# Optimization experiments

Measured on AMD Instinct MI355X. Metric: run time of the kernel, lower is better.

## Reference

```python
import jax, jax.numpy as jnp
import numpy as np

LN_EPS = 1e-5

def _layernorm(x, w, b):
    mu = jnp.mean(x, axis=-1, keepdims=True)
    var = jnp.mean(jnp.square(x - mu), axis=-1, keepdims=True)
    return (x - mu) * jax.lax.rsqrt(var + LN_EPS) * w + b

def setup_inputs() -> dict:
    key = jax.random.key(0)
    ks = jax.random.split(key, 6)
    B, NQ, QD = 8, 576, 4096
    NKV, KVD = 2304, 1024
    s = 0.02
    return {
        "x_q": jax.random.normal(ks[0], (B, NQ, QD), jnp.float32),
        "x_kv": jax.random.normal(ks[1], (B, NKV, KVD), jnp.float32),
        "q_ln_w": jnp.ones((QD,), jnp.float32),
        "q_ln_b": jnp.zeros((QD,), jnp.float32),
        "q_w": jax.random.normal(ks[2], (QD, QD), jnp.float32) * s,
        "q_b": jnp.zeros((QD,), jnp.float32),
        "k_ln_w": jnp.ones((KVD,), jnp.float32),
        "k_ln_b": jnp.zeros((KVD,), jnp.float32),
        "k_w": jax.random.normal(ks[3], (KVD, QD), jnp.float32) * s,
        "k_b": jnp.zeros((QD,), jnp.float32),
        "v_ln_w": jnp.ones((KVD,), jnp.float32),
        "v_ln_b": jnp.zeros((KVD,), jnp.float32),
        "v_w": jax.random.normal(ks[4], (KVD, QD), jnp.float32) * s,
        "v_b": jnp.zeros((QD,), jnp.float32),
    }

def reference(x_q, x_kv, q_ln_w, q_ln_b, q_w, q_b,
              k_ln_w, k_ln_b, k_w, k_b, v_ln_w, v_ln_b, v_w, v_b):
    B, NQ, QD = x_q.shape
    hw = int(round(x_kv.shape[1] ** 0.5))          # 48
    KVD = x_kv.shape[-1]
    patch_num = int(round(NQ ** 0.5))              # 24
    patch_size = hw // patch_num                   # 2
    # 'b (h w) d -> b h w d' then group into patch_num x patch_num windows
    kv = x_kv.reshape(B, hw, hw, KVD)
    kv = kv.reshape(B, patch_num, patch_size, patch_num, patch_size, KVD)
    kv = kv.transpose(0, 1, 3, 2, 4, 5).reshape(B, patch_num * patch_num, patch_size * patch_size, KVD)
    # projections (LayerNorm + Linear)
    q = _layernorm(x_q, q_ln_w, q_ln_b) @ q_w + q_b            # [B, P2, QD]
    k = _layernorm(kv, k_ln_w, k_ln_b) @ k_w + k_b             # [B, P2, S2, QD]
    v = _layernorm(kv, v_ln_w, v_ln_b) @ v_w + v_b             # [B, P2, S2, QD]
    scale = 1.0 / (QD ** 0.5)
    att = jnp.einsum('bpd,bpsd->bps', q, k) * scale            # [B, P2, S2]
    att = jnp.nan_to_num(att)
    att = jax.nn.softmax(att, axis=-1)
    feat = jnp.einsum('bps,bpsd->bpd', att, v)                 # [B, P2, QD]
    return (x_q, feat)
```

## Files before the change

kernel.cpp:

```cpp
#include <hip/hip_runtime.h>
#include <cstdint>
#include <cstddef>


typedef __attribute__((ext_vector_type(8))) short short8;
typedef __attribute__((ext_vector_type(4))) float f32x4;

#define DEV __device__ __forceinline__

DEV unsigned short f2bf(float f) {
  union { float f; unsigned u; } x; x.f = f;
  unsigned r = x.u + 0x7fffu + ((x.u >> 16) & 1u);
  return (unsigned short)(r >> 16);
}
DEV float bf2f(unsigned short u) {
  union { unsigned u; float f; } x; x.u = ((unsigned)u) << 16;
  return x.f;
}

DEV void gload16(const void* g, void* l) {
  __builtin_amdgcn_global_load_lds(
      (const __attribute__((address_space(1))) unsigned int*)g,
      (__attribute__((address_space(3))) unsigned int*)l, 16, 0, 0);
}

template <bool PARTIAL, bool HAS_BIAS>
__global__ __launch_bounds__(512, 2) void gemm_nt(
    const unsigned short* __restrict__ A, const unsigned short* __restrict__ Bm,
    void* __restrict__ Cv, const float* __restrict__ bias, int M, int N,
    int Kfull, int Kchunk) {
  __shared__ __align__(16) unsigned short lds_a[2][256 * 64];
  __shared__ __align__(16) unsigned short lds_b[2][256 * 64];
  const int t = threadIdx.x;
  const int l = t & 63;
  const int wid = t >> 6;

  int bx = blockIdx.x, by = blockIdx.y;
  {
    const int nbx = gridDim.x, nby = gridDim.y;
    const int nwg = nbx * nby;
    int flat = by * nbx + bx;
    flat = (flat & 7) * (nwg >> 3) + (flat >> 3);
    bx = flat % nbx;
    by = flat / nbx;
  }
  const long brow = (long)bx * 256;
  const long bcol = (long)by * 256;
  const int z = blockIdx.z;
  const int k0 = z * Kchunk;

  const int srow0 = t >> 3;
  const int gsrc = (t & 7) ^ ((t >> 3) & 7);
  const unsigned short* aS[4];
  const unsigned short* bS[4];
#pragma unroll
  for (int j = 0; j < 4; ++j) {
    const long row = srow0 + 64 * j;
    aS[j] = A + (brow + row) * (long)Kfull + k0 + gsrc * 8;
    bS[j] = Bm + (bcol + row) * (long)Kfull + k0 + gsrc * 8;
  }
  const int dOff = t * 8;

  const int wr = wid >> 2, wc = wid & 3;
  const int fr = l & 15;
  const int xr = fr & 7;
  const int gq0 = l >> 4;

  f32x4 acc[8][4] = {};

#pragma unroll
  for (int j = 0; j < 4; ++j) {
    gload16(aS[j], &lds_a[0][dOff + 4096 * j]);
    gload16(bS[j], &lds_b[0][dOff + 4096 * j]);
  }
  asm volatile("s_waitcnt vmcnt(0)" ::: "memory");
  __syncthreads();

  int cur = 0;
  for (int kt = 0; kt < Kchunk; kt += 64) {
    const int nxt = cur ^ 1;
    if (kt + 64 < Kchunk) {
#pragma unroll
      for (int j = 0; j < 4; ++j) {
        gload16(aS[j] + kt + 64, &lds_a[nxt][dOff + 4096 * j]);
        gload16(bS[j] + kt + 64, &lds_b[nxt][dOff + 4096 * j]);
      }
    }
#pragma unroll
    for (int ks = 0; ks < 2; ++ks) {
      const int gx = ((ks * 4 + gq0) ^ xr) * 8;
      short8 bfr[4];
#pragma unroll
      for (int ni = 0; ni < 4; ++ni)
        bfr[ni] =
            *(const short8*)&lds_b[cur][(wc * 64 + ni * 16 + fr) * 64 + gx];
#pragma unroll
      for (int mi = 0; mi < 8; ++mi) {
        const short8 af =
            *(const short8*)&lds_a[cur][(wr * 128 + mi * 16 + fr) * 64 + gx];
#pragma unroll
        for (int ni = 0; ni < 4; ++ni)
          acc[mi][ni] = __builtin_amdgcn_mfma_f32_16x16x32_bf16(
              af, bfr[ni], acc[mi][ni], 0, 0, 0);
      }
    }
    asm volatile("s_waitcnt vmcnt(0)" ::: "memory");
    __syncthreads();
    cur = nxt;
  }

  const int crow = (l >> 4) * 4;
  unsigned short* Cpart =
      PARTIAL ? ((unsigned short*)Cv + (size_t)z * M * (size_t)N) : nullptr;
#pragma unroll
  for (int ni = 0; ni < 4; ++ni) {
    const long col = bcol + wc * 64 + ni * 16 + fr;
    const float bv = (!PARTIAL && HAS_BIAS) ? bias[col] : 0.0f;
#pragma unroll
    for (int mi = 0; mi < 8; ++mi) {
#pragma unroll
      for (int r = 0; r < 4; ++r) {
        const long row = brow + wr * 128 + mi * 16 + crow + r;
        const float v = acc[mi][ni][r] + bv;
        if (PARTIAL)
          Cpart[row * (long)N + col] = f2bf(v);
        else
          ((float*)Cv)[row * (long)N + col] = v;
      }
    }
  }
}

__global__ __launch_bounds__(256) void reduce_splits_bf16(
    const unsigned short* __restrict__ part, unsigned short* __restrict__ out,
    int S, size_t MN) {
  size_t i = (size_t)blockIdx.x * 256 + threadIdx.x;
  const size_t n4 = MN / 4;
  const size_t stride = (size_t)gridDim.x * 256;
  for (; i < n4; i += stride) {
    float a0 = 0.f, a1 = 0.f, a2 = 0.f, a3 = 0.f;
    for (int s = 0; s < S; ++s) {
      const ushort4 b = ((const ushort4*)(part + (size_t)s * MN))[i];
      a0 += bf2f(b.x); a1 += bf2f(b.y); a2 += bf2f(b.z); a3 += bf2f(b.w);
    }
    ((ushort4*)out)[i] = make_ushort4(f2bf(a0), f2bf(a1), f2bf(a2), f2bf(a3));
  }
}

__global__ __launch_bounds__(256) void ln_q_kernel(
    const float* __restrict__ x, const float* __restrict__ w,
    const float* __restrict__ b, float* __restrict__ copy_out,
    unsigned short* __restrict__ qn) {
  const int row = blockIdx.x, t = threadIdx.x;
  const float4* xr = (const float4*)(x + (size_t)row * 4096);
  float4 v[4];
  float s = 0.f, s2 = 0.f;
#pragma unroll
  for (int j = 0; j < 4; ++j) {
    v[j] = xr[j * 256 + t];
    s += v[j].x + v[j].y + v[j].z + v[j].w;
    s2 += v[j].x * v[j].x + v[j].y * v[j].y + v[j].z * v[j].z + v[j].w * v[j].w;
  }
#pragma unroll
  for (int off = 32; off; off >>= 1) {
    s += __shfl_xor(s, off);
    s2 += __shfl_xor(s2, off);
  }
  __shared__ float red[8];
  if ((t & 63) == 0) { red[t >> 6] = s; red[4 + (t >> 6)] = s2; }
  __syncthreads();
  s = red[0] + red[1] + red[2] + red[3];
  s2 = red[4] + red[5] + red[6] + red[7];
  const float mu = s * (1.f / 4096.f);
  const float rstd = rsqrtf(s2 * (1.f / 4096.f) - mu * mu + 1e-5f);
  float4* co = (float4*)(copy_out + (size_t)row * 4096);
  unsigned short* qr = qn + (size_t)row * 4096;
#pragma unroll
  for (int j = 0; j < 4; ++j) {
    co[j * 256 + t] = v[j];
    const int c = (j * 256 + t) * 4;
    const float4 wv = *(const float4*)(w + c);
    const float4 bv = *(const float4*)(b + c);
    ushort4 o = make_ushort4(f2bf((v[j].x - mu) * rstd * wv.x + bv.x),
                             f2bf((v[j].y - mu) * rstd * wv.y + bv.y),
                             f2bf((v[j].z - mu) * rstd * wv.z + bv.z),
                             f2bf((v[j].w - mu) * rstd * wv.w + bv.w));
    *(ushort4*)(qr + c) = o;
  }
}

__global__ __launch_bounds__(256) void ln_kv_kernel(
    const float* __restrict__ x, unsigned short* __restrict__ h) {
  const int row = blockIdx.x, t = threadIdx.x;
  const float4 v = ((const float4*)(x + (size_t)row * 1024))[t];
  float s = v.x + v.y + v.z + v.w;
  float s2 = v.x * v.x + v.y * v.y + v.z * v.z + v.w * v.w;
#pragma unroll
  for (int off = 32; off; off >>= 1) {
    s += __shfl_xor(s, off);
    s2 += __shfl_xor(s2, off);
  }
  __shared__ float red[8];
  if ((t & 63) == 0) { red[t >> 6] = s; red[4 + (t >> 6)] = s2; }
  __syncthreads();
  s = red[0] + red[1] + red[2] + red[3];
  s2 = red[4] + red[5] + red[6] + red[7];
  const float mu = s * (1.f / 1024.f);
  const float rstd = rsqrtf(s2 * (1.f / 1024.f) - mu * mu + 1e-5f);
  *(ushort4*)(h + (size_t)row * 1024 + t * 4) =
      make_ushort4(f2bf((v.x - mu) * rstd), f2bf((v.y - mu) * rstd),
                   f2bf((v.z - mu) * rstd), f2bf((v.w - mu) * rstd));
}

__global__ __launch_bounds__(256) void conv_bf16(
    const float* __restrict__ src, unsigned short* __restrict__ dst, int n4) {
  int i = blockIdx.x * 256 + threadIdx.x;
  const int stride = gridDim.x * 256;
  for (; i < n4; i += stride) {
    const float4 v = ((const float4*)src)[i];
    ((ushort4*)dst)[i] = make_ushort4(f2bf(v.x), f2bf(v.y), f2bf(v.z), f2bf(v.w));
  }
}

__global__ __launch_bounds__(256) void conv_kw_qkb(
    const float* __restrict__ kw, const float* __restrict__ qb,
    unsigned short* __restrict__ kwb, float* __restrict__ qkb) {
  const int c = blockIdx.x, t = threadIdx.x;
  const float4* kr = (const float4*)(kw + (size_t)c * 4096);
  const float4* q4 = (const float4*)qb;
  ushort4* ko = (ushort4*)(kwb + (size_t)c * 4096);
  float s = 0.f;
#pragma unroll
  for (int j = 0; j < 4; ++j) {
    const float4 a = q4[j * 256 + t], b = kr[j * 256 + t];
    ko[j * 256 + t] = make_ushort4(f2bf(b.x), f2bf(b.y), f2bf(b.z), f2bf(b.w));
    s += a.x * b.x + a.y * b.y + a.z * b.z + a.w * b.w;
  }
#pragma unroll
  for (int off = 32; off; off >>= 1) s += __shfl_xor(s, off);
  __shared__ float red[4];
  if ((t & 63) == 0) red[t >> 6] = s;
  __syncthreads();
  if (t == 0) qkb[c] = red[0] + red[1] + red[2] + red[3];
}

__global__ void transpose_conv(const float* __restrict__ src,
                               const float* __restrict__ vlnw,
                               unsigned short* __restrict__ dst) {
  __shared__ float tile[32][33];
  const int n0 = blockIdx.x * 32, k0 = blockIdx.y * 32;
  const int tx = threadIdx.x, ty = threadIdx.y;
#pragma unroll
  for (int i = 0; i < 32; i += 8)
    tile[ty + i][tx] = src[(size_t)(k0 + ty + i) * 4096 + n0 + tx];
  __syncthreads();
  const float vw_ = vlnw[k0 + tx];
#pragma unroll
  for (int i = 0; i < 32; i += 8)
    dst[(size_t)(n0 + ty + i) * 1024 + k0 + tx] = f2bf(tile[tx][ty + i] * vw_);
}

__global__ __launch_bounds__(256) void vb_fold(const float* __restrict__ vw_,
                                               const float* __restrict__ vlnb,
                                               const float* __restrict__ vb,
                                               float* __restrict__ bias2) {
  const int nl = threadIdx.x & 63;
  const int seg = threadIdx.x >> 6;
  const int n = blockIdx.x * 64 + nl;
  float s = 0.f;
  for (int d = seg * 256; d < seg * 256 + 256; ++d)
    s += vlnb[d] * vw_[(size_t)d * 4096 + n];
  __shared__ float red[4][64];
  red[seg][nl] = s;
  __syncthreads();
  if (seg == 0)
    bias2[n] = vb[n] + red[0][nl] + red[1][nl] + red[2][nl] + red[3][nl];
}

__global__ __launch_bounds__(256) void att_fused(
    const unsigned short* __restrict__ part, int S, size_t PMN,
    const float* __restrict__ qkb, const float* __restrict__ klnw,
    const unsigned short* __restrict__ h, unsigned short* __restrict__ mix) {
  const int m = blockIdx.x;
  const int b = m / 576, p = m % 576;
  const int py = p / 24, px = p % 24;
  const int t = threadIdx.x, w = t >> 6, l = t & 63;
  const int c = t * 4;
  const size_t off = (size_t)m * 1024 + c;

  float4 q = *(const float4*)(qkb + c);
  for (int s = 0; s < S; ++s) {
    const ushort4 pp = *(const ushort4*)(part + (size_t)s * PMN + off);
    q.x += bf2f(pp.x); q.y += bf2f(pp.y); q.z += bf2f(pp.z); q.w += bf2f(pp.w);
  }
  const float4 kw4 = *(const float4*)(klnw + c);
  q.x *= kw4.x; q.y *= kw4.y; q.z *= kw4.z; q.w *= kw4.w;

  size_t rows[4];
#pragma unroll
  for (int s = 0; s < 4; ++s)
    rows[s] = ((size_t)b * 2304 + (size_t)(py * 2 + (s >> 1)) * 48 +
               (px * 2 + (s & 1))) * 1024;

  float hv[4][4];
  float dot[4];
#pragma unroll
  for (int s = 0; s < 4; ++s) {
    const ushort4 h4 = *(const ushort4*)(h + rows[s] + c);
    hv[s][0] = bf2f(h4.x); hv[s][1] = bf2f(h4.y);
    hv[s][2] = bf2f(h4.z); hv[s][3] = bf2f(h4.w);
    dot[s] = q.x * hv[s][0] + q.y * hv[s][1] + q.z * hv[s][2] + q.w * hv[s][3];
  }
#pragma unroll
  for (int s = 0; s < 4; ++s)
#pragma unroll
    for (int o = 32; o; o >>= 1) dot[s] += __shfl_xor(dot[s], o);

  __shared__ float red[4][4];
  if (l == 0) {
#pragma unroll
    for (int s = 0; s < 4; ++s) red[w][s] = dot[s];
  }
  __syncthreads();
  float lg[4];
#pragma unroll
  for (int s = 0; s < 4; ++s)
    lg[s] = (red[0][s] + red[1][s] + red[2][s] + red[3][s]) * 0.015625f;
  const float mx = fmaxf(fmaxf(lg[0], lg[1]), fmaxf(lg[2], lg[3]));
  float e[4];
#pragma unroll
  for (int s = 0; s < 4; ++s) e[s] = __expf(lg[s] - mx);
  const float inv = 1.f / (e[0] + e[1] + e[2] + e[3]);

  float a0 = 0.f, a1 = 0.f, a2 = 0.f, a3 = 0.f;
#pragma unroll
  for (int s = 0; s < 4; ++s) {
    const float at = e[s] * inv;
    a0 += at * hv[s][0];
    a1 += at * hv[s][1];
    a2 += at * hv[s][2];
    a3 += at * hv[s][3];
  }
  *(ushort4*)(mix + off) =
      make_ushort4(f2bf(a0), f2bf(a1), f2bf(a2), f2bf(a3));
}

extern "C" void kernel_launch(void* const* d_in, const int* in_sizes, int n_in,
                              void* d_out, int out_size, void* d_ws,
                              size_t ws_size, hipStream_t stream) {
  const float* x_q = (const float*)d_in[0];
  const float* x_kv = (const float*)d_in[1];
  const float* q_ln_w = (const float*)d_in[2];
  const float* q_ln_b = (const float*)d_in[3];
  const float* q_w = (const float*)d_in[4];
  const float* q_b = (const float*)d_in[5];
  const float* k_ln_w = (const float*)d_in[6];
  const float* k_w = (const float*)d_in[8];
  const float* v_ln_w = (const float*)d_in[10];
  const float* v_ln_b = (const float*)d_in[11];
  const float* v_w = (const float*)d_in[12];
  const float* v_b = (const float*)d_in[13];

  char* ws = (char*)d_ws;
  unsigned short* qn = (unsigned short*)(ws);
  unsigned short* h = (unsigned short*)(ws + 37748736);
  float* bias2 = (float*)(ws + 75497472);
  unsigned short* qwb = (unsigned short*)(ws + 113246208);
  unsigned short* kwb = (unsigned short*)(ws + 146800640);
  unsigned short* Wt = (unsigned short*)(ws + 155189248);
  unsigned short* vwT = (unsigned short*)(ws + 163577856);
  float* qkbv = (float*)(ws + 190840832);
  unsigned short* mix = (unsigned short*)(ws + 190844928);
  unsigned short* part = (unsigned short*)(ws + 200282112);

  const size_t MN_W = (size_t)1024 * 4096;
  const size_t MN_QK = (size_t)4608 * 1024;
  int splitW = 1, splitQK = 1;
  if (ws_size >= 200282112ull + 4 * MN_QK * 2) { splitW = 4; splitQK = 4; }
  else if (ws_size >= 200282112ull + 2 * MN_QK * 2) { splitW = 2; splitQK = 2; }

  float* out0 = (float*)d_out;
  float* out1 = out0 + (size_t)4608 * 4096;

  ln_q_kernel<<<4608, 256, 0, stream>>>(x_q, q_ln_w, q_ln_b, out0, qn);
  ln_kv_kernel<<<18432, 256, 0, stream>>>(x_kv, h);
  conv_bf16<<<4096, 256, 0, stream>>>(q_w, qwb, 4096 * 4096 / 4);
  conv_kw_qkb<<<1024, 256, 0, stream>>>(k_w, q_b, kwb, qkbv);
  transpose_conv<<<dim3(128, 32), dim3(32, 8), 0, stream>>>(v_w, v_ln_w, vwT);
  vb_fold<<<64, 256, 0, stream>>>(v_w, v_ln_b, v_b, bias2);

  gemm_nt<true, false><<<dim3(4, 16, splitW), 512, 0, stream>>>(
      kwb, qwb, part, nullptr, 1024, 4096, 4096, 4096 / splitW);
  reduce_splits_bf16<<<2048, 256, 0, stream>>>(part, Wt, splitW, MN_W);

  gemm_nt<true, false><<<dim3(18, 4, splitQK), 512, 0, stream>>>(
      qn, Wt, part, nullptr, 4608, 1024, 4096, 4096 / splitQK);
  att_fused<<<4608, 256, 0, stream>>>(part, splitQK, MN_QK, qkbv, k_ln_w, h,
                                      mix);

  gemm_nt<false, true><<<dim3(18, 16, 1), 512, 0, stream>>>(
      mix, vwT, out1, bias2, 4608, 4096, 1024, 1024);
}
```

Before: 599.5 us.

## Shrink GEMM tiles to 128x128 with 4 waves and single-buffered LDS

The GEMM kernel moves from 256x256 tiles with 8 waves and double-buffered LDS to 128x128 tiles with 4 waves and a single LDS buffer. Each tile now loads, waits and then computes, with no prefetch. The grids grow accordingly, and the W-product split-K drops from 4 to 2. The aim is more workgroups and higher occupancy per CU, at the cost of less data reuse per tile and exposed global-load latency.

```diff
diff --git a/kernel.cpp b/kernel.cpp
--- a/kernel.cpp
+++ b/kernel.cpp
@@ -25,15 +25,15 @@
 }
 
 template <bool PARTIAL, bool HAS_BIAS>
-__global__ __launch_bounds__(512, 2) void gemm_nt(
+__global__ __launch_bounds__(256, 2) void gemm_nt(
     const unsigned short* __restrict__ A, const unsigned short* __restrict__ Bm,
     void* __restrict__ Cv, const float* __restrict__ bias, int M, int N,
     int Kfull, int Kchunk) {
-  __shared__ __align__(16) unsigned short lds_a[2][256 * 64];
-  __shared__ __align__(16) unsigned short lds_b[2][256 * 64];
+  __shared__ __align__(16) unsigned short lds_a[128 * 64];
+  __shared__ __align__(16) unsigned short lds_b[128 * 64];
   const int t = threadIdx.x;
   const int l = t & 63;
-  const int wid = t >> 6;
+  const int w = t >> 6;
 
   int bx = blockIdx.x, by = blockIdx.y;
   {
@@ -44,8 +44,8 @@
     bx = flat % nbx;
     by = flat / nbx;
   }
-  const long brow = (long)bx * 256;
-  const long bcol = (long)by * 256;
+  const long brow = (long)bx * 128;
+  const long bcol = (long)by * 128;
   const int z = blockIdx.z;
   const int k0 = z * Kchunk;
 
@@ -53,60 +53,50 @@
   const int gsrc = (t & 7) ^ ((t >> 3) & 7);
   const unsigned short* aS[4];
   const unsigned short* bS[4];
+  unsigned short* aD[4];
+  unsigned short* bD[4];
 #pragma unroll
   for (int j = 0; j < 4; ++j) {
-    const long row = srow0 + 64 * j;
+    const long row = srow0 + 32 * j;
     aS[j] = A + (brow + row) * (long)Kfull + k0 + gsrc * 8;
     bS[j] = Bm + (bcol + row) * (long)Kfull + k0 + gsrc * 8;
-  }
-  const int dOff = t * 8;
-
-  const int wr = wid >> 2, wc = wid & 3;
+    aD[j] = lds_a + (t + 256 * j) * 8;
+    bD[j] = lds_b + (t + 256 * j) * 8;
+  }
+
+  const int wr = w >> 1, wc = w & 1;
   const int fr = l & 15;
   const int xr = fr & 7;
   const int gq0 = l >> 4;
 
-  f32x4 acc[8][4] = {};
-
-#pragma unroll
-  for (int j = 0; j < 4; ++j) {
-    gload16(aS[j], &lds_a[0][dOff + 4096 * j]);
-    gload16(bS[j], &lds_b[0][dOff + 4096 * j]);
-  }
-  asm volatile("s_waitcnt vmcnt(0)" ::: "memory");
-  __syncthreads();
-
-  int cur = 0;
+  f32x4 acc[4][4] = {};
+
   for (int kt = 0; kt < Kchunk; kt += 64) {
-    const int nxt = cur ^ 1;
-    if (kt + 64 < Kchunk) {
-#pragma unroll
-      for (int j = 0; j < 4; ++j) {
-        gload16(aS[j] + kt + 64, &lds_a[nxt][dOff + 4096 * j]);
-        gload16(bS[j] + kt + 64, &lds_b[nxt][dOff + 4096 * j]);
-      }
-    }
-#pragma unroll
-    for (int ks = 0; ks < 2; ++ks) {
-      const int gx = ((ks * 4 + gq0) ^ xr) * 8;
-      short8 bfr[4];
-#pragma unroll
-      for (int ni = 0; ni < 4; ++ni)
-        bfr[ni] =
-            *(const short8*)&lds_b[cur][(wc * 64 + ni * 16 + fr) * 64 + gx];
-#pragma unroll
-      for (int mi = 0; mi < 8; ++mi) {
-        const short8 af =
-            *(const short8*)&lds_a[cur][(wr * 128 + mi * 16 + fr) * 64 + gx];
-#pragma unroll
-        for (int ni = 0; ni < 4; ++ni)
-          acc[mi][ni] = __builtin_amdgcn_mfma_f32_16x16x32_bf16(
-              af, bfr[ni], acc[mi][ni], 0, 0, 0);
-      }
+    __syncthreads();
+#pragma unroll
+    for (int j = 0; j < 4; ++j) {
+      gload16(aS[j] + kt, aD[j]);
+      gload16(bS[j] + kt, bD[j]);
     }
     asm volatile("s_waitcnt vmcnt(0)" ::: "memory");
     __syncthreads();
-    cur = nxt;
+#pragma unroll
+    for (int ks = 0; ks < 2; ++ks) {
+      const int gx = ((ks * 4 + gq0) ^ xr) * 8;
+      short8 af[4], bfr[4];
+#pragma unroll
+      for (int mi = 0; mi < 4; ++mi)
+        af[mi] = *(const short8*)&lds_a[(wr * 64 + mi * 16 + fr) * 64 + gx];
+#pragma unroll
+      for (int ni = 0; ni < 4; ++ni)
+        bfr[ni] = *(const short8*)&lds_b[(wc * 64 + ni * 16 + fr) * 64 + gx];
+#pragma unroll
+      for (int mi = 0; mi < 4; ++mi)
+#pragma unroll
+        for (int ni = 0; ni < 4; ++ni)
+          acc[mi][ni] = __builtin_amdgcn_mfma_f32_16x16x32_bf16(
+              af[mi], bfr[ni], acc[mi][ni], 0, 0, 0);
+    }
   }
 
   const int crow = (l >> 4) * 4;
@@ -117,10 +107,10 @@
     const long col = bcol + wc * 64 + ni * 16 + fr;
     const float bv = (!PARTIAL && HAS_BIAS) ? bias[col] : 0.0f;
 #pragma unroll
-    for (int mi = 0; mi < 8; ++mi) {
+    for (int mi = 0; mi < 4; ++mi) {
 #pragma unroll
       for (int r = 0; r < 4; ++r) {
-        const long row = brow + wr * 128 + mi * 16 + crow + r;
+        const long row = brow + wr * 64 + mi * 16 + crow + r;
         const float v = acc[mi][ni][r] + bv;
         if (PARTIAL)
           Cpart[row * (long)N + col] = f2bf(v);
@@ -376,7 +366,7 @@
   const size_t MN_W = (size_t)1024 * 4096;
   const size_t MN_QK = (size_t)4608 * 1024;
   int splitW = 1, splitQK = 1;
-  if (ws_size >= 200282112ull + 4 * MN_QK * 2) { splitW = 4; splitQK = 4; }
+  if (ws_size >= 200282112ull + 4 * MN_QK * 2) { splitW = 2; splitQK = 4; }
   else if (ws_size >= 200282112ull + 2 * MN_QK * 2) { splitW = 2; splitQK = 2; }
 
   float* out0 = (float*)d_out;
@@ -389,15 +379,15 @@
   transpose_conv<<<dim3(128, 32), dim3(32, 8), 0, stream>>>(v_w, v_ln_w, vwT);
   vb_fold<<<64, 256, 0, stream>>>(v_w, v_ln_b, v_b, bias2);
 
-  gemm_nt<true, false><<<dim3(4, 16, splitW), 512, 0, stream>>>(
+  gemm_nt<true, false><<<dim3(8, 32, splitW), 256, 0, stream>>>(
       kwb, qwb, part, nullptr, 1024, 4096, 4096, 4096 / splitW);
   reduce_splits_bf16<<<2048, 256, 0, stream>>>(part, Wt, splitW, MN_W);
 
-  gemm_nt<true, false><<<dim3(18, 4, splitQK), 512, 0, stream>>>(
+  gemm_nt<true, false><<<dim3(36, 8, splitQK), 256, 0, stream>>>(
       qn, Wt, part, nullptr, 4608, 1024, 4096, 4096 / splitQK);
   att_fused<<<4608, 256, 0, stream>>>(part, splitQK, MN_QK, qkbv, k_ln_w, h,
                                       mix);
 
-  gemm_nt<false, true><<<dim3(18, 16, 1), 512, 0, stream>>>(
+  gemm_nt<false, true><<<dim3(36, 32, 1), 256, 0, stream>>>(
       mix, vwT, out1, bias2, 4608, 4096, 1024, 1024);
 }
```

Measured after the change: 553.9 us. 7.6% less time.
